# Performance work log

Hardware: AMD Instinct MI355X
Metric: run time of the kernel (lower is better)

## Reference

```python
import jax, jax.numpy as jnp
import numpy as np

F_IN, F_OUT, N_HEADS = 64, 256, 4
HEAD_DIM = F_OUT // N_HEADS


def setup_inputs() -> dict:
    key = jax.random.key(0)
    ks = jax.random.split(key, 9)
    s_in = 1.0 / np.sqrt(F_IN)
    s_out = 1.0 / np.sqrt(F_OUT)
    return {
        "x": jax.random.normal(ks[0], (4, 32, F_IN, 512), dtype=jnp.float32),
        "Wq": jax.random.normal(ks[1], (F_IN, F_OUT), dtype=jnp.float32) * s_in,
        "bq": jax.random.normal(ks[2], (F_OUT,), dtype=jnp.float32) * 0.01,
        "Wk": jax.random.normal(ks[3], (F_IN, F_OUT), dtype=jnp.float32) * s_in,
        "bk": jax.random.normal(ks[4], (F_OUT,), dtype=jnp.float32) * 0.01,
        "Wv": jax.random.normal(ks[5], (F_IN, F_OUT), dtype=jnp.float32) * s_in,
        "bv": jax.random.normal(ks[6], (F_OUT,), dtype=jnp.float32) * 0.01,
        "Wo": jax.random.normal(ks[7], (F_OUT, F_OUT), dtype=jnp.float32) * s_out,
        "bo": jax.random.normal(ks[8], (F_OUT,), dtype=jnp.float32) * 0.01,
    }


def reference(x, Wq, bq, Wk, bk, Wv, bv, Wo, bo):
    B, N, Fdim, T = x.shape
    xp = jnp.transpose(x, (0, 1, 3, 2))  # [B, N, T, F]
    q = xp @ Wq + bq  # [B, N, T, f_out]
    k = xp @ Wk + bk
    v = xp @ Wv + bv
    # split f_out into heads: [B, N, T, H, hd]
    q = q.reshape(B, N, T, N_HEADS, HEAD_DIM)
    k = k.reshape(B, N, T, N_HEADS, HEAD_DIM)
    v = v.reshape(B, N, T, N_HEADS, HEAD_DIM)
    scale = 1.0 / np.sqrt(HEAD_DIM)
    # full TxT score matrix per (batch, node, head), as in the original
    scores = jnp.einsum("bnqhd,bnkhd->bnhqk", q, k) * scale
    attn = jax.nn.softmax(scores, axis=-1)
    out = jnp.einsum("bnhqk,bnkhd->bnqhd", attn, v)  # [B, N, T, H, hd]
    out = out.reshape(B, N, T, F_OUT)  # head-concat along feature dim
    out = out @ Wo + bo  # fc_out; dropout is identity at inference
    return jnp.transpose(out, (0, 1, 3, 2))  # [B, N, f_out, T]
```

## Files before the change

### kernel.cpp

```cpp
#include <hip/hip_runtime.h>

constexpr int kT = 512;
constexpr int kF = 64;
constexpr int kC = 256;
constexpr int kH = 4;
constexpr int kHD = 64;
constexpr int kBN = 128;

typedef __attribute__((ext_vector_type(4))) float f32x4;
typedef __attribute__((ext_vector_type(8))) short s16x8;
typedef __attribute__((ext_vector_type(4))) unsigned int u32x4;

__device__ inline unsigned short f2bf(float f) {
  unsigned int u = __float_as_uint(f);
  u += 0x7fff + ((u >> 16) & 1);
  return (unsigned short)(u >> 16);
}

__device__ inline unsigned int cvt_pk(float a, float b) {
  unsigned int w;
  asm("v_cvt_pk_bf16_f32 %0, %1, %2" : "=v"(w) : "v"(a), "v"(b));
  return w;
}

__device__ inline float max3f(float a, float b, float c) {
  return fmaxf(fmaxf(a, b), c);
}

__device__ inline float exp2_hw(float x) {
  float r;
  asm("v_exp_f32 %0, %1" : "=v"(r) : "v"(x));
  return r;
}

__global__ __launch_bounds__(256) void k_prep(
    const float* __restrict__ Wq, const float* __restrict__ Wk,
    const float* __restrict__ Wv, const float* __restrict__ Wo,
    unsigned short* __restrict__ WB, unsigned short* __restrict__ WoT) {
  int i = blockIdx.x * 256 + threadIdx.x;
  const int total = 768 * 64 + 256 * 256;
  for (; i < total; i += gridDim.x * 256) {
    if (i < 768 * 64) {
      int c = i >> 6, f = i & 63;
      int arr = c >> 8, cc = c & 255;
      const float* W = (arr == 0) ? Wq : (arr == 1) ? Wk : Wv;
      WB[i] = f2bf(W[f * 256 + cc]);
    } else {
      int j = i - 768 * 64;
      int co = j >> 8, c = j & 255;
      WoT[j] = f2bf(Wo[c * 256 + co]);
    }
  }
}

__global__ __launch_bounds__(1024, 4) void k_fattn(
    const float* __restrict__ x, const unsigned short* __restrict__ WB,
    const float* __restrict__ bq, const float* __restrict__ bk,
    const float* __restrict__ bv, unsigned short* __restrict__ Aw) {
  __shared__ __align__(16) unsigned char smem[149504];
  unsigned char* Kl = smem;
  unsigned char* VtB = smem + 65536;
  unsigned char* xCb = smem + 131072;

  const int tid = threadIdx.x;
  const int bid = blockIdx.x;
  const int orig = (bid & 7) * 64 + (bid >> 3);
  const int lbn = orig >> 2;
  const int h = orig & 3;
  const int lane = tid & 63, wid = tid >> 6;
  const int lr = lane & 15, lg = lane >> 4;
  const int swz = (lr & 7) << 4;

  const float kQscale = 0.180336880111120426f;
  const unsigned short* WBq = WB + (size_t)(h * 64) * 64;
  const unsigned short* WBk = WB + (size_t)(256 + h * 64) * 64;
  const unsigned short* WBv = WB + (size_t)(512 + h * 64) * 64;

#define XFRAG(r, c) (const s16x8*)(xCb + (r) * 144 + \
    (((c) * 2) ^ ((((r) >> 2) & 7) << 4)))

  s16x8 qf[2][2];

  for (int tch = 0; tch < 4; ++tch) {
    __syncthreads();
    const float* xb = x + (size_t)lbn * kF * kT + tch * 128;
#pragma unroll
    for (int it = 0; it < 2; ++it) {
      int idx = tid + it * 1024;
      int f = idx >> 5, t4 = idx & 31;
      float4 v = *(const float4*)(xb + f * kT + t4 * 4);
      unsigned int wlo = cvt_pk(v.x, v.y);
      unsigned int whi = cvt_pk(v.z, v.w);
      const int fb = f * 2;
      const int colb = (fb & 15) | ((((fb >> 4) ^ (t4 & 7))) << 4);
      unsigned char* rp = xCb + (t4 * 4) * 144 + colb;
      *(unsigned short*)(rp + 0 * 144) = (unsigned short)wlo;
      *(unsigned short*)(rp + 1 * 144) = (unsigned short)(wlo >> 16);
      *(unsigned short*)(rp + 2 * 144) = (unsigned short)whi;
      *(unsigned short*)(rp + 3 * 144) = (unsigned short)(whi >> 16);
    }
    __syncthreads();

#pragma unroll
    for (int j = 0; j < 4; ++j) {
      const int tau = wid * 4 + j;
      const int isV = tau >> 5;
      const int tl = tau & 31;
      const int ct = tl >> 3, tt = tl & 7;
      const unsigned short* Wsrc = isV ? WBv : WBk;
      s16x8 af0 = *(const s16x8*)(Wsrc + (ct * 16 + lr) * 64 + lg * 8);
      s16x8 af1 = *(const s16x8*)(Wsrc + (ct * 16 + lr) * 64 + 32 + lg * 8);
      s16x8 bf0 = *XFRAG(tt * 16 + lr, lg * 8);
      s16x8 bf1 = *XFRAG(tt * 16 + lr, 32 + lg * 8);
      if (!isV) {
        f32x4 a = {0.f, 0.f, 0.f, 0.f};
        a = __builtin_amdgcn_mfma_f32_16x16x32_bf16(af0, bf0, a, 0, 0, 0);
        a = __builtin_amdgcn_mfma_f32_16x16x32_bf16(af1, bf1, a, 0, 0, 0);
        const int dbase = ct * 16 + lg * 4;
        const int t = tch * 128 + tt * 16 + lr;
        uint2 pk;
        pk.x = cvt_pk(a[0] + bk[h * 64 + dbase + 0],
                      a[1] + bk[h * 64 + dbase + 1]);
        pk.y = cvt_pk(a[2] + bk[h * 64 + dbase + 2],
                      a[3] + bk[h * 64 + dbase + 3]);
        *(uint2*)(Kl + ((t * 128 + dbase * 2) ^ ((t & 7) << 4))) = pk;
      } else {
        f32x4 a = {0.f, 0.f, 0.f, 0.f};
        a = __builtin_amdgcn_mfma_f32_16x16x32_bf16(bf0, af0, a, 0, 0, 0);
        a = __builtin_amdgcn_mfma_f32_16x16x32_bf16(bf1, af1, a, 0, 0, 0);
        const int d = ct * 16 + lr;
        const float bias = bv[h * 64 + d];
        const int t0 = tch * 128 + tt * 16 + lg * 4;
        const int pos0 = ((t0 >> 5) << 5) | (((t0 >> 2) & 3) << 3) |
                         (((t0 >> 4) & 1) << 2);
        uint2 pk;
        pk.x = cvt_pk(a[0] + bias, a[1] + bias);
        pk.y = cvt_pk(a[2] + bias, a[3] + bias);
        *(uint2*)(VtB + ((d * 1024 + pos0 * 2) ^ ((d & 7) << 4))) = pk;
      }
    }

    if ((wid >> 2) == tch) {
      f32x4 qa[2][4];
#pragma unroll
      for (int qt = 0; qt < 2; ++qt) {
        const int ttq = (wid & 3) * 2 + qt;
#pragma unroll
        for (int ct = 0; ct < 4; ++ct) {
          s16x8 af0 = *(const s16x8*)(WBq + (ct * 16 + lr) * 64 + lg * 8);
          s16x8 af1 = *(const s16x8*)(WBq + (ct * 16 + lr) * 64 + 32 + lg * 8);
          s16x8 bf0 = *XFRAG(ttq * 16 + lr, lg * 8);
          s16x8 bf1 = *XFRAG(ttq * 16 + lr, 32 + lg * 8);
          f32x4 a = {0.f, 0.f, 0.f, 0.f};
          a = __builtin_amdgcn_mfma_f32_16x16x32_bf16(af0, bf0, a, 0, 0, 0);
          a = __builtin_amdgcn_mfma_f32_16x16x32_bf16(af1, bf1, a, 0, 0, 0);
          const int dbase = ct * 16 + lg * 4;
#pragma unroll
          for (int r = 0; r < 4; ++r)
            a[r] = (a[r] + bq[h * 64 + dbase + r]) * kQscale;
          qa[qt][ct] = a;
        }
      }
      const int sel = lg >> 1;
#pragma unroll
      for (int qt = 0; qt < 2; ++qt)
#pragma unroll
        for (int half = 0; half < 2; ++half) {
          unsigned int w[4];
#pragma unroll
          for (int i2 = 0; i2 < 4; ++i2) {
            const int r0 = (i2 & 1) * 2;
            const int lgp = (lg & 1) * 2 + (i2 >> 1);
            const int src = lgp * 16 + lr;
            float loA = __shfl(qa[qt][half * 2 + 0][r0], src);
            float hiA = __shfl(qa[qt][half * 2 + 1][r0], src);
            float loB = __shfl(qa[qt][half * 2 + 0][r0 + 1], src);
            float hiB = __shfl(qa[qt][half * 2 + 1][r0 + 1], src);
            w[i2] = cvt_pk(sel ? hiA : loA, sel ? hiB : loB);
          }
          qf[qt][half] =
              __builtin_bit_cast(s16x8, (u32x4){w[0], w[1], w[2], w[3]});
        }
    }
  }
  __syncthreads();
#undef XFRAG

  unsigned short* Ab = Aw + (size_t)lbn * kT * kC + h * kHD;
  const int qbase = wid * 32;

  f32x4 o0[4] = {{0,0,0,0},{0,0,0,0},{0,0,0,0},{0,0,0,0}};
  f32x4 o1[4] = {{0,0,0,0},{0,0,0,0},{0,0,0,0},{0,0,0,0}};
  float m0 = -3e38f, m1 = -3e38f, l0 = 0.f, l1 = 0.f;

  const int koff = (lg * 16) ^ swz;
  const unsigned char* kp0 = Kl + lr * 128 + koff;
  const unsigned char* kp1 = Kl + lr * 128 + (koff ^ 64);
  const unsigned char* vp0 = VtB + lr * 1024 + ((lg * 16) ^ swz);
  const unsigned char* vp1 = VtB + lr * 1024 + (((lg * 16) ^ 64) ^ swz);

  unsigned int w0[8], w1[8];

#define SOFTMAX_QT(sa, m, l, o, w)                                            \
  {                                                                           \
    float g0 = max3f(sa[0][0], sa[0][1], sa[0][2]);                           \
    float g1 = max3f(sa[0][3], sa[1][0], sa[1][1]);                           \
    float g2 = max3f(sa[1][2], sa[1][3], sa[2][0]);                           \
    float g3 = max3f(sa[2][1], sa[2][2], sa[2][3]);                           \
    float g4 = max3f(sa[3][0], sa[3][1], sa[3][2]);                           \
    float tm = fmaxf(max3f(g0, g1, g2), max3f(g3, g4, sa[3][3]));             \
    if (__any(tm > m + 8.0f)) {                                               \
      tm = fmaxf(tm, __shfl_xor(tm, 16));                                     \
      tm = fmaxf(tm, __shfl_xor(tm, 32));                                     \
      float mn = fmaxf(m, tm);                                                \
      float al = exp2_hw(m - mn);                                             \
      m = mn;                                                                 \
      l *= al;                                                                \
      float aq0 = __shfl(al, (lane & 48) | (lg * 4 + 0));                     \
      float aq1 = __shfl(al, (lane & 48) | (lg * 4 + 1));                     \
      float aq2 = __shfl(al, (lane & 48) | (lg * 4 + 2));                     \
      float aq3 = __shfl(al, (lane & 48) | (lg * 4 + 3));                     \
      _Pragma("unroll")                                                       \
      for (int dt = 0; dt < 4; ++dt) {                                        \
        o[dt][0] *= aq0; o[dt][1] *= aq1;                                     \
        o[dt][2] *= aq2; o[dt][3] *= aq3;                                     \
      }                                                                       \
    }                                                                         \
    _Pragma("unroll")                                                         \
    for (int s = 0; s < 4; ++s) {                                             \
      float e0 = exp2_hw(sa[s][0] - m);                                       \
      float e1 = exp2_hw(sa[s][1] - m);                                       \
      float e2 = exp2_hw(sa[s][2] - m);                                       \
      float e3 = exp2_hw(sa[s][3] - m);                                       \
      l += (e0 + e1) + (e2 + e3);                                             \
      w[2*s]   = cvt_pk(e0, e1);                                              \
      w[2*s+1] = cvt_pk(e2, e3);                                              \
    }                                                                         \
  }

  for (int kc = 0; kc < 8; ++kc) {
    f32x4 sa0[4], sa1[4];
#pragma unroll
    for (int s = 0; s < 4; ++s) {
      s16x8 kf0 = *(const s16x8*)(kp0 + s * 2048);
      s16x8 kf1 = *(const s16x8*)(kp1 + s * 2048);
      f32x4 z0 = {0.f, 0.f, 0.f, 0.f};
      z0 = __builtin_amdgcn_mfma_f32_16x16x32_bf16(kf0, qf[0][0], z0, 0, 0, 0);
      z0 = __builtin_amdgcn_mfma_f32_16x16x32_bf16(kf1, qf[0][1], z0, 0, 0, 0);
      sa0[s] = z0;
      f32x4 z1 = {0.f, 0.f, 0.f, 0.f};
      z1 = __builtin_amdgcn_mfma_f32_16x16x32_bf16(kf0, qf[1][0], z1, 0, 0, 0);
      z1 = __builtin_amdgcn_mfma_f32_16x16x32_bf16(kf1, qf[1][1], z1, 0, 0, 0);
      sa1[s] = z1;
    }
    kp0 += 8192;
    kp1 += 8192;

    s16x8 vb0[4], vb1[4];
#pragma unroll
    for (int dt = 0; dt < 4; ++dt) {
      vb0[dt] = *(const s16x8*)(vp0 + dt * 16384);
      vb1[dt] = *(const s16x8*)(vp1 + dt * 16384);
    }
    vp0 += 128;
    vp1 += 128;

    SOFTMAX_QT(sa0, m0, l0, o0, w0)
    SOFTMAX_QT(sa1, m1, l1, o1, w1)

    s16x8 pa00 = __builtin_bit_cast(s16x8, (u32x4){w0[0], w0[1], w0[2], w0[3]});
    s16x8 pa01 = __builtin_bit_cast(s16x8, (u32x4){w0[4], w0[5], w0[6], w0[7]});
    s16x8 pa10 = __builtin_bit_cast(s16x8, (u32x4){w1[0], w1[1], w1[2], w1[3]});
    s16x8 pa11 = __builtin_bit_cast(s16x8, (u32x4){w1[4], w1[5], w1[6], w1[7]});

#pragma unroll
    for (int dt = 0; dt < 4; ++dt) {
      o0[dt] = __builtin_amdgcn_mfma_f32_16x16x32_bf16(pa00, vb0[dt], o0[dt], 0, 0, 0);
      o1[dt] = __builtin_amdgcn_mfma_f32_16x16x32_bf16(pa10, vb0[dt], o1[dt], 0, 0, 0);
    }
#pragma unroll
    for (int dt = 0; dt < 4; ++dt) {
      o0[dt] = __builtin_amdgcn_mfma_f32_16x16x32_bf16(pa01, vb1[dt], o0[dt], 0, 0, 0);
      o1[dt] = __builtin_amdgcn_mfma_f32_16x16x32_bf16(pa11, vb1[dt], o1[dt], 0, 0, 0);
    }
  }
#undef SOFTMAX_QT

#pragma unroll
  for (int qt = 0; qt < 2; ++qt) {
    float l = (qt == 0) ? l0 : l1;
    f32x4* o = (qt == 0) ? o0 : o1;
    float l2 = l + __shfl_xor(l, 16);
    float lr4 = l2 + __shfl_xor(l2, 32);
    float li0 = 1.0f / __shfl(lr4, (lane & 48) | (lg * 4 + 0));
    float li1 = 1.0f / __shfl(lr4, (lane & 48) | (lg * 4 + 1));
    float li2 = 1.0f / __shfl(lr4, (lane & 48) | (lg * 4 + 2));
    float li3 = 1.0f / __shfl(lr4, (lane & 48) | (lg * 4 + 3));
    const int qb = qbase + qt * 16;
#pragma unroll
    for (int r = 0; r < 4; ++r) {
      float li = (r == 0) ? li0 : (r == 1) ? li1 : (r == 2) ? li2 : li3;
      unsigned short* orow = Ab + (size_t)(qb + lg * 4 + r) * kC;
      unsigned int wa = cvt_pk(o[0][r] * li, o[1][r] * li);
      unsigned int wb = cvt_pk(o[2][r] * li, o[3][r] * li);
      orow[0 * 16 + lr] = (unsigned short)wa;
      orow[1 * 16 + lr] = (unsigned short)(wa >> 16);
      orow[2 * 16 + lr] = (unsigned short)wb;
      orow[3 * 16 + lr] = (unsigned short)(wb >> 16);
    }
  }
}

__global__ __launch_bounds__(512) void k_proj(
    const unsigned short* __restrict__ Aw, const unsigned short* __restrict__ WoT,
    const float* __restrict__ bo, float* __restrict__ out) {
  __shared__ __align__(16) unsigned char Al[128 * 512];

  const int tid = threadIdx.x;
  const int lbn = blockIdx.x >> 2;
  const int tch = blockIdx.x & 3;
  const int t0 = tch * 128;

  const uint4* Asrc = (const uint4*)(Aw + ((size_t)lbn * kT + t0) * kC);
#pragma unroll
  for (int i = 0; i < 8; ++i) {
    int idx = tid + i * 512;
    int trow = idx >> 5, cc = idx & 31;
    *(uint4*)(Al + ((trow * 512 + cc * 16) ^ ((trow & 7) << 4))) = Asrc[idx];
  }
  __syncthreads();

  const int lane = tid & 63, wid = tid >> 6;
  const int lr = lane & 15, lg = lane >> 4;
  const int swz = (lr & 7) << 4;
  const int tb = (wid >> 2) * 64;
  const int cob = (wid & 3) * 64;

  float* ob = out + (size_t)lbn * kC * kT;

  for (int ci = 0; ci < 4; ++ci) {
    const int co0 = cob + ci * 16;
    s16x8 af[8];
#pragma unroll
    for (int kc = 0; kc < 8; ++kc)
      af[kc] = *(const s16x8*)(WoT + (size_t)(co0 + lr) * 256 + kc * 32 + lg * 8);
    float b4[4];
#pragma unroll
    for (int r = 0; r < 4; ++r) b4[r] = bo[co0 + lg * 4 + r];

#pragma unroll
    for (int tj = 0; tj < 4; ++tj) {
      const unsigned char* ap = Al + (tb + tj * 16 + lr) * 512;
      f32x4 acc = {0.f, 0.f, 0.f, 0.f};
#pragma unroll
      for (int kc = 0; kc < 8; ++kc) {
        s16x8 bfr = *(const s16x8*)(ap + ((kc * 64 + lg * 16) ^ swz));
        acc = __builtin_amdgcn_mfma_f32_16x16x32_bf16(af[kc], bfr, acc, 0, 0, 0);
      }
      int t = t0 + tb + tj * 16 + lr;
#pragma unroll
      for (int r = 0; r < 4; ++r)
        ob[(size_t)(co0 + lg * 4 + r) * kT + t] = acc[r] + b4[r];
    }
  }
}

extern "C" void kernel_launch(void* const* d_in, const int* in_sizes, int n_in,
                              void* d_out, int out_size, void* d_ws, size_t ws_size,
                              hipStream_t stream) {
  const float* x  = (const float*)d_in[0];
  const float* Wq = (const float*)d_in[1];
  const float* bq = (const float*)d_in[2];
  const float* Wk = (const float*)d_in[3];
  const float* bk = (const float*)d_in[4];
  const float* Wv = (const float*)d_in[5];
  const float* bv = (const float*)d_in[6];
  const float* Wo = (const float*)d_in[7];
  const float* bo = (const float*)d_in[8];
  float* out = (float*)d_out;

  const size_t wElems = 768 * 64 + 256 * 256;
  const size_t aBytes = (size_t)kBN * kT * kC * 2;
  if (ws_size < wElems * 2 + aBytes) return;

  unsigned short* WB  = (unsigned short*)d_ws;
  unsigned short* WoT = WB + 768 * 64;
  unsigned short* A   = WB + wElems;

  k_prep<<<dim3(448), dim3(256), 0, stream>>>(Wq, Wk, Wv, Wo, WB, WoT);
  k_fattn<<<dim3(kBN * kH), dim3(1024), 0, stream>>>(x, WB, bq, bk, bv, A);
  k_proj<<<dim3(kBN * 4), dim3(512), 0, stream>>>(A, WoT, bo, out);
}
```

Baseline: 120.7 us.

## Overlap attention chunks with K/V projection and prefetch x tiles

Q is now computed up front by each wave straight from global x, without going through the shared x tile. The attention loop over key chunks is interleaved with the per-tch K/V projection, so chunks already written to LDS are consumed while later chunks are still being produced. The next x tile is prefetched into registers one iteration ahead. This aims to hide projection and global-load latency behind attention MFMA work, at the cost of strided uncoalesced global reads for Q and higher register pressure.

```diff
diff --git a/kernel.cpp b/kernel.cpp
--- a/kernel.cpp
+++ b/kernel.cpp
@@ -75,29 +75,194 @@
   const unsigned short* WBq = WB + (size_t)(h * 64) * 64;
   const unsigned short* WBk = WB + (size_t)(256 + h * 64) * 64;
   const unsigned short* WBv = WB + (size_t)(512 + h * 64) * 64;
+  const float* xb0 = x + (size_t)lbn * kF * kT;
 
 #define XFRAG(r, c) (const s16x8*)(xCb + (r) * 144 + \
     (((c) * 2) ^ ((((r) >> 2) & 7) << 4)))
 
+  const int qbase = wid * 32;
+
   s16x8 qf[2][2];
+  {
+    f32x4 qa[2][4];
+#pragma unroll
+    for (int qt = 0; qt < 2; ++qt) {
+      const int tq = qbase + qt * 16 + lr;
+      s16x8 bfr[2];
+#pragma unroll
+      for (int kk = 0; kk < 2; ++kk) {
+        unsigned int wv[4];
+#pragma unroll
+        for (int jp = 0; jp < 4; ++jp) {
+          float fa = xb0[(size_t)(kk * 32 + lg * 8 + 2 * jp) * kT + tq];
+          float fb = xb0[(size_t)(kk * 32 + lg * 8 + 2 * jp + 1) * kT + tq];
+          wv[jp] = cvt_pk(fa, fb);
+        }
+        bfr[kk] = __builtin_bit_cast(s16x8, (u32x4){wv[0], wv[1], wv[2], wv[3]});
+      }
+#pragma unroll
+      for (int ct = 0; ct < 4; ++ct) {
+        s16x8 af0 = *(const s16x8*)(WBq + (ct * 16 + lr) * 64 + lg * 8);
+        s16x8 af1 = *(const s16x8*)(WBq + (ct * 16 + lr) * 64 + 32 + lg * 8);
+        f32x4 a = {0.f, 0.f, 0.f, 0.f};
+        a = __builtin_amdgcn_mfma_f32_16x16x32_bf16(af0, bfr[0], a, 0, 0, 0);
+        a = __builtin_amdgcn_mfma_f32_16x16x32_bf16(af1, bfr[1], a, 0, 0, 0);
+        const int dbase = ct * 16 + lg * 4;
+#pragma unroll
+        for (int r = 0; r < 4; ++r)
+          a[r] = (a[r] + bq[h * 64 + dbase + r]) * kQscale;
+        qa[qt][ct] = a;
+      }
+    }
+    const int sel = lg >> 1;
+#pragma unroll
+    for (int qt = 0; qt < 2; ++qt)
+#pragma unroll
+      for (int half = 0; half < 2; ++half) {
+        unsigned int w[4];
+#pragma unroll
+        for (int i2 = 0; i2 < 4; ++i2) {
+          const int r0 = (i2 & 1) * 2;
+          const int lgp = (lg & 1) * 2 + (i2 >> 1);
+          const int src = lgp * 16 + lr;
+          float loA = __shfl(qa[qt][half * 2 + 0][r0], src);
+          float hiA = __shfl(qa[qt][half * 2 + 1][r0], src);
+          float loB = __shfl(qa[qt][half * 2 + 0][r0 + 1], src);
+          float hiB = __shfl(qa[qt][half * 2 + 1][r0 + 1], src);
+          w[i2] = cvt_pk(sel ? hiA : loA, sel ? hiB : loB);
+        }
+        qf[qt][half] =
+            __builtin_bit_cast(s16x8, (u32x4){w[0], w[1], w[2], w[3]});
+      }
+  }
+
+  unsigned short* Ab = Aw + (size_t)lbn * kT * kC + h * kHD;
+  f32x4 o0[4] = {{0,0,0,0},{0,0,0,0},{0,0,0,0},{0,0,0,0}};
+  f32x4 o1[4] = {{0,0,0,0},{0,0,0,0},{0,0,0,0},{0,0,0,0}};
+  float m0 = -3e38f, m1 = -3e38f, l0 = 0.f, l1 = 0.f;
+  unsigned int w0[8], w1[8];
+
+  const int koff = (lg * 16) ^ swz;
+  const unsigned char* kb0 = Kl + lr * 128 + koff;
+  const unsigned char* kb1 = Kl + lr * 128 + (koff ^ 64);
+  const unsigned char* vbp0 = VtB + lr * 1024 + ((lg * 16) ^ swz);
+  const unsigned char* vbp1 = VtB + lr * 1024 + (((lg * 16) ^ 64) ^ swz);
+
+#define SOFTMAX_QT(sa, m, l, o, w)                                            \
+  {                                                                           \
+    float g0 = max3f(sa[0][0], sa[0][1], sa[0][2]);                           \
+    float g1 = max3f(sa[0][3], sa[1][0], sa[1][1]);                           \
+    float g2 = max3f(sa[1][2], sa[1][3], sa[2][0]);                           \
+    float g3 = max3f(sa[2][1], sa[2][2], sa[2][3]);                           \
+    float g4 = max3f(sa[3][0], sa[3][1], sa[3][2]);                           \
+    float tm = fmaxf(max3f(g0, g1, g2), max3f(g3, g4, sa[3][3]));             \
+    if (__any(tm > m + 8.0f)) {                                               \
+      tm = fmaxf(tm, __shfl_xor(tm, 16));                                     \
+      tm = fmaxf(tm, __shfl_xor(tm, 32));                                     \
+      float mn = fmaxf(m, tm);                                                \
+      float al = exp2_hw(m - mn);                                             \
+      m = mn;                                                                 \
+      l *= al;                                                                \
+      float aq0 = __shfl(al, (lane & 48) | (lg * 4 + 0));                     \
+      float aq1 = __shfl(al, (lane & 48) | (lg * 4 + 1));                     \
+      float aq2 = __shfl(al, (lane & 48) | (lg * 4 + 2));                     \
+      float aq3 = __shfl(al, (lane & 48) | (lg * 4 + 3));                     \
+      _Pragma("unroll")                                                       \
+      for (int dt = 0; dt < 4; ++dt) {                                        \
+        o[dt][0] *= aq0; o[dt][1] *= aq1;                                     \
+        o[dt][2] *= aq2; o[dt][3] *= aq3;                                     \
+      }                                                                       \
+    }                                                                         \
+    _Pragma("unroll")                                                         \
+    for (int s = 0; s < 4; ++s) {                                             \
+      float e0 = exp2_hw(sa[s][0] - m);                                       \
+      float e1 = exp2_hw(sa[s][1] - m);                                       \
+      float e2 = exp2_hw(sa[s][2] - m);                                       \
+      float e3 = exp2_hw(sa[s][3] - m);                                       \
+      l += (e0 + e1) + (e2 + e3);                                             \
+      w[2*s]   = cvt_pk(e0, e1);                                              \
+      w[2*s+1] = cvt_pk(e2, e3);                                              \
+    }                                                                         \
+  }
+
+#define ATTN_KC(kc)                                                           \
+  {                                                                           \
+    const unsigned char* kp0_ = kb0 + (kc) * 8192;                            \
+    const unsigned char* kp1_ = kb1 + (kc) * 8192;                            \
+    f32x4 sa0[4], sa1[4];                                                     \
+    _Pragma("unroll")                                                         \
+    for (int s = 0; s < 4; ++s) {                                             \
+      s16x8 kf0 = *(const s16x8*)(kp0_ + s * 2048);                           \
+      s16x8 kf1 = *(const s16x8*)(kp1_ + s * 2048);                           \
+      f32x4 z0 = {0.f, 0.f, 0.f, 0.f};                                        \
+      z0 = __builtin_amdgcn_mfma_f32_16x16x32_bf16(kf0, qf[0][0], z0, 0,0,0); \
+      z0 = __builtin_amdgcn_mfma_f32_16x16x32_bf16(kf1, qf[0][1], z0, 0,0,0); \
+      sa0[s] = z0;                                                            \
+      f32x4 z1 = {0.f, 0.f, 0.f, 0.f};                                        \
+      z1 = __builtin_amdgcn_mfma_f32_16x16x32_bf16(kf0, qf[1][0], z1, 0,0,0); \
+      z1 = __builtin_amdgcn_mfma_f32_16x16x32_bf16(kf1, qf[1][1], z1, 0,0,0); \
+      sa1[s] = z1;                                                            \
+    }                                                                         \
+    s16x8 vv0[4], vv1[4];                                                     \
+    _Pragma("unroll")                                                         \
+    for (int dt = 0; dt < 4; ++dt) {                                          \
+      vv0[dt] = *(const s16x8*)(vbp0 + (kc) * 128 + dt * 16384);              \
+      vv1[dt] = *(const s16x8*)(vbp1 + (kc) * 128 + dt * 16384);              \
+    }                                                                         \
+    SOFTMAX_QT(sa0, m0, l0, o0, w0)                                           \
+    SOFTMAX_QT(sa1, m1, l1, o1, w1)                                           \
+    s16x8 pa00 = __builtin_bit_cast(s16x8, (u32x4){w0[0],w0[1],w0[2],w0[3]}); \
+    s16x8 pa01 = __builtin_bit_cast(s16x8, (u32x4){w0[4],w0[5],w0[6],w0[7]}); \
+    s16x8 pa10 = __builtin_bit_cast(s16x8, (u32x4){w1[0],w1[1],w1[2],w1[3]}); \
+    s16x8 pa11 = __builtin_bit_cast(s16x8, (u32x4){w1[4],w1[5],w1[6],w1[7]}); \
+    _Pragma("unroll")                                                         \
+    for (int dt = 0; dt < 4; ++dt) {                                          \
+      o0[dt] = __builtin_amdgcn_mfma_f32_16x16x32_bf16(pa00, vv0[dt], o0[dt], 0,0,0); \
+      o1[dt] = __builtin_amdgcn_mfma_f32_16x16x32_bf16(pa10, vv0[dt], o1[dt], 0,0,0); \
+    }                                                                         \
+    _Pragma("unroll")                                                         \
+    for (int dt = 0; dt < 4; ++dt) {                                          \
+      o0[dt] = __builtin_amdgcn_mfma_f32_16x16x32_bf16(pa01, vv1[dt], o0[dt], 0,0,0); \
+      o1[dt] = __builtin_amdgcn_mfma_f32_16x16x32_bf16(pa11, vv1[dt], o1[dt], 0,0,0); \
+    }                                                                         \
+  }
+
+  const int sf0 = tid >> 5;
+  const int st4 = tid & 31;
+  const int sf1 = (tid + 1024) >> 5;
+
+  float4 pf0 = *(const float4*)(xb0 + (size_t)sf0 * kT + st4 * 4);
+  float4 pf1 = *(const float4*)(xb0 + (size_t)sf1 * kT + st4 * 4);
 
   for (int tch = 0; tch < 4; ++tch) {
     __syncthreads();
-    const float* xb = x + (size_t)lbn * kF * kT + tch * 128;
-#pragma unroll
-    for (int it = 0; it < 2; ++it) {
-      int idx = tid + it * 1024;
-      int f = idx >> 5, t4 = idx & 31;
-      float4 v = *(const float4*)(xb + f * kT + t4 * 4);
-      unsigned int wlo = cvt_pk(v.x, v.y);
-      unsigned int whi = cvt_pk(v.z, v.w);
-      const int fb = f * 2;
-      const int colb = (fb & 15) | ((((fb >> 4) ^ (t4 & 7))) << 4);
-      unsigned char* rp = xCb + (t4 * 4) * 144 + colb;
+
+    {
+      unsigned int wlo = cvt_pk(pf0.x, pf0.y);
+      unsigned int whi = cvt_pk(pf0.z, pf0.w);
+      int colb = ((sf0 * 2) & 15) | (((((sf0 * 2) >> 4) ^ (st4 & 7))) << 4);
+      unsigned char* rp = xCb + (st4 * 4) * 144 + colb;
       *(unsigned short*)(rp + 0 * 144) = (unsigned short)wlo;
       *(unsigned short*)(rp + 1 * 144) = (unsigned short)(wlo >> 16);
       *(unsigned short*)(rp + 2 * 144) = (unsigned short)whi;
       *(unsigned short*)(rp + 3 * 144) = (unsigned short)(whi >> 16);
+      wlo = cvt_pk(pf1.x, pf1.y);
+      whi = cvt_pk(pf1.z, pf1.w);
+      colb = ((sf1 * 2) & 15) | (((((sf1 * 2) >> 4) ^ (st4 & 7))) << 4);
+      rp = xCb + (st4 * 4) * 144 + colb;
+      *(unsigned short*)(rp + 0 * 144) = (unsigned short)wlo;
+      *(unsigned short*)(rp + 1 * 144) = (unsigned short)(wlo >> 16);
+      *(unsigned short*)(rp + 2 * 144) = (unsigned short)whi;
+      *(unsigned short*)(rp + 3 * 144) = (unsigned short)(whi >> 16);
+    }
+    if (tch < 3) {
+      const float* xb = xb0 + (tch + 1) * 128;
+      pf0 = *(const float4*)(xb + (size_t)sf0 * kT + st4 * 4);
+      pf1 = *(const float4*)(xb + (size_t)sf1 * kT + st4 * 4);
+    }
+    if (tch > 0) {
+      ATTN_KC(2 * tch - 2)
+      ATTN_KC(2 * tch - 1)
     }
     __syncthreads();
 
@@ -139,152 +304,14 @@
         *(uint2*)(VtB + ((d * 1024 + pos0 * 2) ^ ((d & 7) << 4))) = pk;
       }
     }
-
-    if ((wid >> 2) == tch) {
-      f32x4 qa[2][4];
-#pragma unroll
-      for (int qt = 0; qt < 2; ++qt) {
-        const int ttq = (wid & 3) * 2 + qt;
-#pragma unroll
-        for (int ct = 0; ct < 4; ++ct) {
-          s16x8 af0 = *(const s16x8*)(WBq + (ct * 16 + lr) * 64 + lg * 8);
-          s16x8 af1 = *(const s16x8*)(WBq + (ct * 16 + lr) * 64 + 32 + lg * 8);
-          s16x8 bf0 = *XFRAG(ttq * 16 + lr, lg * 8);
-          s16x8 bf1 = *XFRAG(ttq * 16 + lr, 32 + lg * 8);
-          f32x4 a = {0.f, 0.f, 0.f, 0.f};
-          a = __builtin_amdgcn_mfma_f32_16x16x32_bf16(af0, bf0, a, 0, 0, 0);
-          a = __builtin_amdgcn_mfma_f32_16x16x32_bf16(af1, bf1, a, 0, 0, 0);
-          const int dbase = ct * 16 + lg * 4;
-#pragma unroll
-          for (int r = 0; r < 4; ++r)
-            a[r] = (a[r] + bq[h * 64 + dbase + r]) * kQscale;
-          qa[qt][ct] = a;
-        }
-      }
-      const int sel = lg >> 1;
-#pragma unroll
-      for (int qt = 0; qt < 2; ++qt)
-#pragma unroll
-        for (int half = 0; half < 2; ++half) {
-          unsigned int w[4];
-#pragma unroll
-          for (int i2 = 0; i2 < 4; ++i2) {
-            const int r0 = (i2 & 1) * 2;
-            const int lgp = (lg & 1) * 2 + (i2 >> 1);
-            const int src = lgp * 16 + lr;
-            float loA = __shfl(qa[qt][half * 2 + 0][r0], src);
-            float hiA = __shfl(qa[qt][half * 2 + 1][r0], src);
-            float loB = __shfl(qa[qt][half * 2 + 0][r0 + 1], src);
-            float hiB = __shfl(qa[qt][half * 2 + 1][r0 + 1], src);
-            w[i2] = cvt_pk(sel ? hiA : loA, sel ? hiB : loB);
-          }
-          qf[qt][half] =
-              __builtin_bit_cast(s16x8, (u32x4){w[0], w[1], w[2], w[3]});
-        }
-    }
   }
   __syncthreads();
+
+  ATTN_KC(6)
+  ATTN_KC(7)
+#undef ATTN_KC
+#undef SOFTMAX_QT
 #undef XFRAG
-
-  unsigned short* Ab = Aw + (size_t)lbn * kT * kC + h * kHD;
-  const int qbase = wid * 32;
-
-  f32x4 o0[4] = {{0,0,0,0},{0,0,0,0},{0,0,0,0},{0,0,0,0}};
-  f32x4 o1[4] = {{0,0,0,0},{0,0,0,0},{0,0,0,0},{0,0,0,0}};
-  float m0 = -3e38f, m1 = -3e38f, l0 = 0.f, l1 = 0.f;
-
-  const int koff = (lg * 16) ^ swz;
-  const unsigned char* kp0 = Kl + lr * 128 + koff;
-  const unsigned char* kp1 = Kl + lr * 128 + (koff ^ 64);
-  const unsigned char* vp0 = VtB + lr * 1024 + ((lg * 16) ^ swz);
-  const unsigned char* vp1 = VtB + lr * 1024 + (((lg * 16) ^ 64) ^ swz);
-
-  unsigned int w0[8], w1[8];
-
-#define SOFTMAX_QT(sa, m, l, o, w)                                            \
-  {                                                                           \
-    float g0 = max3f(sa[0][0], sa[0][1], sa[0][2]);                           \
-    float g1 = max3f(sa[0][3], sa[1][0], sa[1][1]);                           \
-    float g2 = max3f(sa[1][2], sa[1][3], sa[2][0]);                           \
-    float g3 = max3f(sa[2][1], sa[2][2], sa[2][3]);                           \
-    float g4 = max3f(sa[3][0], sa[3][1], sa[3][2]);                           \
-    float tm = fmaxf(max3f(g0, g1, g2), max3f(g3, g4, sa[3][3]));             \
-    if (__any(tm > m + 8.0f)) {                                               \
-      tm = fmaxf(tm, __shfl_xor(tm, 16));                                     \
-      tm = fmaxf(tm, __shfl_xor(tm, 32));                                     \
-      float mn = fmaxf(m, tm);                                                \
-      float al = exp2_hw(m - mn);                                             \
-      m = mn;                                                                 \
-      l *= al;                                                                \
-      float aq0 = __shfl(al, (lane & 48) | (lg * 4 + 0));                     \
-      float aq1 = __shfl(al, (lane & 48) | (lg * 4 + 1));                     \
-      float aq2 = __shfl(al, (lane & 48) | (lg * 4 + 2));                     \
-      float aq3 = __shfl(al, (lane & 48) | (lg * 4 + 3));                     \
-      _Pragma("unroll")                                                       \
-      for (int dt = 0; dt < 4; ++dt) {                                        \
-        o[dt][0] *= aq0; o[dt][1] *= aq1;                                     \
-        o[dt][2] *= aq2; o[dt][3] *= aq3;                                     \
-      }                                                                       \
-    }                                                                         \
-    _Pragma("unroll")                                                         \
-    for (int s = 0; s < 4; ++s) {                                             \
-      float e0 = exp2_hw(sa[s][0] - m);                                       \
-      float e1 = exp2_hw(sa[s][1] - m);                                       \
-      float e2 = exp2_hw(sa[s][2] - m);                                       \
-      float e3 = exp2_hw(sa[s][3] - m);                                       \
-      l += (e0 + e1) + (e2 + e3);                                             \
-      w[2*s]   = cvt_pk(e0, e1);                                              \
-      w[2*s+1] = cvt_pk(e2, e3);                                              \
-    }                                                                         \
-  }
-
-  for (int kc = 0; kc < 8; ++kc) {
-    f32x4 sa0[4], sa1[4];
-#pragma unroll
-    for (int s = 0; s < 4; ++s) {
-      s16x8 kf0 = *(const s16x8*)(kp0 + s * 2048);
-      s16x8 kf1 = *(const s16x8*)(kp1 + s * 2048);
-      f32x4 z0 = {0.f, 0.f, 0.f, 0.f};
-      z0 = __builtin_amdgcn_mfma_f32_16x16x32_bf16(kf0, qf[0][0], z0, 0, 0, 0);
-      z0 = __builtin_amdgcn_mfma_f32_16x16x32_bf16(kf1, qf[0][1], z0, 0, 0, 0);
-      sa0[s] = z0;
-      f32x4 z1 = {0.f, 0.f, 0.f, 0.f};
-      z1 = __builtin_amdgcn_mfma_f32_16x16x32_bf16(kf0, qf[1][0], z1, 0, 0, 0);
-      z1 = __builtin_amdgcn_mfma_f32_16x16x32_bf16(kf1, qf[1][1], z1, 0, 0, 0);
-      sa1[s] = z1;
-    }
-    kp0 += 8192;
-    kp1 += 8192;
-
-    s16x8 vb0[4], vb1[4];
-#pragma unroll
-    for (int dt = 0; dt < 4; ++dt) {
-      vb0[dt] = *(const s16x8*)(vp0 + dt * 16384);
-      vb1[dt] = *(const s16x8*)(vp1 + dt * 16384);
-    }
-    vp0 += 128;
-    vp1 += 128;
-
-    SOFTMAX_QT(sa0, m0, l0, o0, w0)
-    SOFTMAX_QT(sa1, m1, l1, o1, w1)
-
-    s16x8 pa00 = __builtin_bit_cast(s16x8, (u32x4){w0[0], w0[1], w0[2], w0[3]});
-    s16x8 pa01 = __builtin_bit_cast(s16x8, (u32x4){w0[4], w0[5], w0[6], w0[7]});
-    s16x8 pa10 = __builtin_bit_cast(s16x8, (u32x4){w1[0], w1[1], w1[2], w1[3]});
-    s16x8 pa11 = __builtin_bit_cast(s16x8, (u32x4){w1[4], w1[5], w1[6], w1[7]});
-
-#pragma unroll
-    for (int dt = 0; dt < 4; ++dt) {
-      o0[dt] = __builtin_amdgcn_mfma_f32_16x16x32_bf16(pa00, vb0[dt], o0[dt], 0, 0, 0);
-      o1[dt] = __builtin_amdgcn_mfma_f32_16x16x32_bf16(pa10, vb0[dt], o1[dt], 0, 0, 0);
-    }
-#pragma unroll
-    for (int dt = 0; dt < 4; ++dt) {
-      o0[dt] = __builtin_amdgcn_mfma_f32_16x16x32_bf16(pa01, vb1[dt], o0[dt], 0, 0, 0);
-      o1[dt] = __builtin_amdgcn_mfma_f32_16x16x32_bf16(pa11, vb1[dt], o1[dt], 0, 0, 0);
-    }
-  }
-#undef SOFTMAX_QT
 
 #pragma unroll
   for (int qt = 0; qt < 2; ++qt) {
```

After: 200.7 us. 66.4% more time.

## Split attention blocks by query half and stream K/V in two key halves

Applied to the files above, without the earlier changes.

The fused attention kernel now launches twice as many 512-thread blocks, each handling half of the queries for one (batch-node, head). K and V are projected in two 256-key halves into smaller shared buffers, and attention runs over each half before the next is built. Q is computed straight from global x instead of staging it through shared memory. Shared memory per block is roughly halved, which raises occupancy, but every query-half block recomputes the full K and V projection, doubling that work and the x reads, and adds syncs between halves.

```diff
diff --git a/kernel.cpp b/kernel.cpp
--- a/kernel.cpp
+++ b/kernel.cpp
@@ -53,20 +53,21 @@
   }
 }
 
-__global__ __launch_bounds__(1024, 4) void k_fattn(
+__global__ __launch_bounds__(512, 4) void k_fattn(
     const float* __restrict__ x, const unsigned short* __restrict__ WB,
     const float* __restrict__ bq, const float* __restrict__ bk,
     const float* __restrict__ bv, unsigned short* __restrict__ Aw) {
-  __shared__ __align__(16) unsigned char smem[149504];
+  __shared__ __align__(16) unsigned char smem[73728];
   unsigned char* Kl = smem;
-  unsigned char* VtB = smem + 65536;
-  unsigned char* xCb = smem + 131072;
+  unsigned char* VtB = smem + 32768;
+  unsigned char* xCb = smem + 65536;
 
   const int tid = threadIdx.x;
   const int bid = blockIdx.x;
-  const int orig = (bid & 7) * 64 + (bid >> 3);
-  const int lbn = orig >> 2;
-  const int h = orig & 3;
+  const int orig = (bid & 7) * 128 + (bid >> 3);
+  const int lbn = orig >> 3;
+  const int h = (orig >> 1) & 3;
+  const int qhalf = orig & 1;
   const int lane = tid & 63, wid = tid >> 6;
   const int lr = lane & 15, lg = lane >> 4;
   const int swz = (lr & 7) << 4;
@@ -75,131 +76,73 @@
   const unsigned short* WBq = WB + (size_t)(h * 64) * 64;
   const unsigned short* WBk = WB + (size_t)(256 + h * 64) * 64;
   const unsigned short* WBv = WB + (size_t)(512 + h * 64) * 64;
-
-#define XFRAG(r, c) (const s16x8*)(xCb + (r) * 144 + \
-    (((c) * 2) ^ ((((r) >> 2) & 7) << 4)))
+  const float* xb0 = x + (size_t)lbn * kF * kT;
 
   s16x8 qf[2][2];
-
-  for (int tch = 0; tch < 4; ++tch) {
-    __syncthreads();
-    const float* xb = x + (size_t)lbn * kF * kT + tch * 128;
-#pragma unroll
-    for (int it = 0; it < 2; ++it) {
-      int idx = tid + it * 1024;
-      int f = idx >> 5, t4 = idx & 31;
-      float4 v = *(const float4*)(xb + f * kT + t4 * 4);
-      unsigned int wlo = cvt_pk(v.x, v.y);
-      unsigned int whi = cvt_pk(v.z, v.w);
-      const int fb = f * 2;
-      const int colb = (fb & 15) | ((((fb >> 4) ^ (t4 & 7))) << 4);
-      unsigned char* rp = xCb + (t4 * 4) * 144 + colb;
-      *(unsigned short*)(rp + 0 * 144) = (unsigned short)wlo;
-      *(unsigned short*)(rp + 1 * 144) = (unsigned short)(wlo >> 16);
-      *(unsigned short*)(rp + 2 * 144) = (unsigned short)whi;
-      *(unsigned short*)(rp + 3 * 144) = (unsigned short)(whi >> 16);
-    }
-    __syncthreads();
-
-#pragma unroll
-    for (int j = 0; j < 4; ++j) {
-      const int tau = wid * 4 + j;
-      const int isV = tau >> 5;
-      const int tl = tau & 31;
-      const int ct = tl >> 3, tt = tl & 7;
-      const unsigned short* Wsrc = isV ? WBv : WBk;
-      s16x8 af0 = *(const s16x8*)(Wsrc + (ct * 16 + lr) * 64 + lg * 8);
-      s16x8 af1 = *(const s16x8*)(Wsrc + (ct * 16 + lr) * 64 + 32 + lg * 8);
-      s16x8 bf0 = *XFRAG(tt * 16 + lr, lg * 8);
-      s16x8 bf1 = *XFRAG(tt * 16 + lr, 32 + lg * 8);
-      if (!isV) {
+  {
+    f32x4 qa[2][4];
+#pragma unroll
+    for (int qt = 0; qt < 2; ++qt) {
+      const int tq = qhalf * 256 + wid * 32 + qt * 16 + lr;
+      s16x8 bfr[2];
+#pragma unroll
+      for (int kk = 0; kk < 2; ++kk) {
+        unsigned int wv[4];
+#pragma unroll
+        for (int jp = 0; jp < 4; ++jp) {
+          float fa = xb0[(size_t)(kk * 32 + lg * 8 + 2 * jp) * kT + tq];
+          float fb = xb0[(size_t)(kk * 32 + lg * 8 + 2 * jp + 1) * kT + tq];
+          wv[jp] = cvt_pk(fa, fb);
+        }
+        bfr[kk] = __builtin_bit_cast(s16x8, (u32x4){wv[0], wv[1], wv[2], wv[3]});
+      }
+#pragma unroll
+      for (int ct = 0; ct < 4; ++ct) {
+        s16x8 af0 = *(const s16x8*)(WBq + (ct * 16 + lr) * 64 + lg * 8);
+        s16x8 af1 = *(const s16x8*)(WBq + (ct * 16 + lr) * 64 + 32 + lg * 8);
         f32x4 a = {0.f, 0.f, 0.f, 0.f};
-        a = __builtin_amdgcn_mfma_f32_16x16x32_bf16(af0, bf0, a, 0, 0, 0);
-        a = __builtin_amdgcn_mfma_f32_16x16x32_bf16(af1, bf1, a, 0, 0, 0);
+        a = __builtin_amdgcn_mfma_f32_16x16x32_bf16(af0, bfr[0], a, 0, 0, 0);
+        a = __builtin_amdgcn_mfma_f32_16x16x32_bf16(af1, bfr[1], a, 0, 0, 0);
         const int dbase = ct * 16 + lg * 4;
-        const int t = tch * 128 + tt * 16 + lr;
-        uint2 pk;
-        pk.x = cvt_pk(a[0] + bk[h * 64 + dbase + 0],
-                      a[1] + bk[h * 64 + dbase + 1]);
-        pk.y = cvt_pk(a[2] + bk[h * 64 + dbase + 2],
-                      a[3] + bk[h * 64 + dbase + 3]);
-        *(uint2*)(Kl + ((t * 128 + dbase * 2) ^ ((t & 7) << 4))) = pk;
-      } else {
-        f32x4 a = {0.f, 0.f, 0.f, 0.f};
-        a = __builtin_amdgcn_mfma_f32_16x16x32_bf16(bf0, af0, a, 0, 0, 0);
-        a = __builtin_amdgcn_mfma_f32_16x16x32_bf16(bf1, af1, a, 0, 0, 0);
-        const int d = ct * 16 + lr;
-        const float bias = bv[h * 64 + d];
-        const int t0 = tch * 128 + tt * 16 + lg * 4;
-        const int pos0 = ((t0 >> 5) << 5) | (((t0 >> 2) & 3) << 3) |
-                         (((t0 >> 4) & 1) << 2);
-        uint2 pk;
-        pk.x = cvt_pk(a[0] + bias, a[1] + bias);
-        pk.y = cvt_pk(a[2] + bias, a[3] + bias);
-        *(uint2*)(VtB + ((d * 1024 + pos0 * 2) ^ ((d & 7) << 4))) = pk;
-      }
-    }
-
-    if ((wid >> 2) == tch) {
-      f32x4 qa[2][4];
-#pragma unroll
-      for (int qt = 0; qt < 2; ++qt) {
-        const int ttq = (wid & 3) * 2 + qt;
-#pragma unroll
-        for (int ct = 0; ct < 4; ++ct) {
-          s16x8 af0 = *(const s16x8*)(WBq + (ct * 16 + lr) * 64 + lg * 8);
-          s16x8 af1 = *(const s16x8*)(WBq + (ct * 16 + lr) * 64 + 32 + lg * 8);
-          s16x8 bf0 = *XFRAG(ttq * 16 + lr, lg * 8);
-          s16x8 bf1 = *XFRAG(ttq * 16 + lr, 32 + lg * 8);
-          f32x4 a = {0.f, 0.f, 0.f, 0.f};
-          a = __builtin_amdgcn_mfma_f32_16x16x32_bf16(af0, bf0, a, 0, 0, 0);
-          a = __builtin_amdgcn_mfma_f32_16x16x32_bf16(af1, bf1, a, 0, 0, 0);
-          const int dbase = ct * 16 + lg * 4;
-#pragma unroll
-          for (int r = 0; r < 4; ++r)
-            a[r] = (a[r] + bq[h * 64 + dbase + r]) * kQscale;
-          qa[qt][ct] = a;
+#pragma unroll
+        for (int r = 0; r < 4; ++r)
+          a[r] = (a[r] + bq[h * 64 + dbase + r]) * kQscale;
+        qa[qt][ct] = a;
+      }
+    }
+    const int sel = lg >> 1;
+#pragma unroll
+    for (int qt = 0; qt < 2; ++qt)
+#pragma unroll
+      for (int half = 0; half < 2; ++half) {
+        unsigned int w[4];
+#pragma unroll
+        for (int i2 = 0; i2 < 4; ++i2) {
+          const int r0 = (i2 & 1) * 2;
+          const int lgp = (lg & 1) * 2 + (i2 >> 1);
+          const int src = lgp * 16 + lr;
+          float loA = __shfl(qa[qt][half * 2 + 0][r0], src);
+          float hiA = __shfl(qa[qt][half * 2 + 1][r0], src);
+          float loB = __shfl(qa[qt][half * 2 + 0][r0 + 1], src);
+          float hiB = __shfl(qa[qt][half * 2 + 1][r0 + 1], src);
+          w[i2] = cvt_pk(sel ? hiA : loA, sel ? hiB : loB);
         }
-      }
-      const int sel = lg >> 1;
-#pragma unroll
-      for (int qt = 0; qt < 2; ++qt)
-#pragma unroll
-        for (int half = 0; half < 2; ++half) {
-          unsigned int w[4];
-#pragma unroll
-          for (int i2 = 0; i2 < 4; ++i2) {
-            const int r0 = (i2 & 1) * 2;
-            const int lgp = (lg & 1) * 2 + (i2 >> 1);
-            const int src = lgp * 16 + lr;
-            float loA = __shfl(qa[qt][half * 2 + 0][r0], src);
-            float hiA = __shfl(qa[qt][half * 2 + 1][r0], src);
-            float loB = __shfl(qa[qt][half * 2 + 0][r0 + 1], src);
-            float hiB = __shfl(qa[qt][half * 2 + 1][r0 + 1], src);
-            w[i2] = cvt_pk(sel ? hiA : loA, sel ? hiB : loB);
-          }
-          qf[qt][half] =
-              __builtin_bit_cast(s16x8, (u32x4){w[0], w[1], w[2], w[3]});
-        }
-    }
-  }
-  __syncthreads();
-#undef XFRAG
+        qf[qt][half] =
+            __builtin_bit_cast(s16x8, (u32x4){w[0], w[1], w[2], w[3]});
+      }
+  }
 
   unsigned short* Ab = Aw + (size_t)lbn * kT * kC + h * kHD;
-  const int qbase = wid * 32;
-
   f32x4 o0[4] = {{0,0,0,0},{0,0,0,0},{0,0,0,0},{0,0,0,0}};
   f32x4 o1[4] = {{0,0,0,0},{0,0,0,0},{0,0,0,0},{0,0,0,0}};
   float m0 = -3e38f, m1 = -3e38f, l0 = 0.f, l1 = 0.f;
+  unsigned int w0[8], w1[8];
 
   const int koff = (lg * 16) ^ swz;
-  const unsigned char* kp0 = Kl + lr * 128 + koff;
-  const unsigned char* kp1 = Kl + lr * 128 + (koff ^ 64);
-  const unsigned char* vp0 = VtB + lr * 1024 + ((lg * 16) ^ swz);
-  const unsigned char* vp1 = VtB + lr * 1024 + (((lg * 16) ^ 64) ^ swz);
-
-  unsigned int w0[8], w1[8];
+  const unsigned char* kb0 = Kl + lr * 128 + koff;
+  const unsigned char* kb1 = Kl + lr * 128 + (koff ^ 64);
+  const unsigned char* vbp0 = VtB + lr * 512 + ((lg * 16) ^ swz);
+  const unsigned char* vbp1 = VtB + lr * 512 + (((lg * 16) ^ 64) ^ swz);
 
 #define SOFTMAX_QT(sa, m, l, o, w)                                            \
   {                                                                           \
@@ -238,50 +181,109 @@
     }                                                                         \
   }
 
-  for (int kc = 0; kc < 8; ++kc) {
-    f32x4 sa0[4], sa1[4];
-#pragma unroll
-    for (int s = 0; s < 4; ++s) {
-      s16x8 kf0 = *(const s16x8*)(kp0 + s * 2048);
-      s16x8 kf1 = *(const s16x8*)(kp1 + s * 2048);
-      f32x4 z0 = {0.f, 0.f, 0.f, 0.f};
-      z0 = __builtin_amdgcn_mfma_f32_16x16x32_bf16(kf0, qf[0][0], z0, 0, 0, 0);
-      z0 = __builtin_amdgcn_mfma_f32_16x16x32_bf16(kf1, qf[0][1], z0, 0, 0, 0);
-      sa0[s] = z0;
-      f32x4 z1 = {0.f, 0.f, 0.f, 0.f};
-      z1 = __builtin_amdgcn_mfma_f32_16x16x32_bf16(kf0, qf[1][0], z1, 0, 0, 0);
-      z1 = __builtin_amdgcn_mfma_f32_16x16x32_bf16(kf1, qf[1][1], z1, 0, 0, 0);
-      sa1[s] = z1;
-    }
-    kp0 += 8192;
-    kp1 += 8192;
-
-    s16x8 vb0[4], vb1[4];
-#pragma unroll
-    for (int dt = 0; dt < 4; ++dt) {
-      vb0[dt] = *(const s16x8*)(vp0 + dt * 16384);
-      vb1[dt] = *(const s16x8*)(vp1 + dt * 16384);
-    }
-    vp0 += 128;
-    vp1 += 128;
-
-    SOFTMAX_QT(sa0, m0, l0, o0, w0)
-    SOFTMAX_QT(sa1, m1, l1, o1, w1)
-
-    s16x8 pa00 = __builtin_bit_cast(s16x8, (u32x4){w0[0], w0[1], w0[2], w0[3]});
-    s16x8 pa01 = __builtin_bit_cast(s16x8, (u32x4){w0[4], w0[5], w0[6], w0[7]});
-    s16x8 pa10 = __builtin_bit_cast(s16x8, (u32x4){w1[0], w1[1], w1[2], w1[3]});
-    s16x8 pa11 = __builtin_bit_cast(s16x8, (u32x4){w1[4], w1[5], w1[6], w1[7]});
-
-#pragma unroll
-    for (int dt = 0; dt < 4; ++dt) {
-      o0[dt] = __builtin_amdgcn_mfma_f32_16x16x32_bf16(pa00, vb0[dt], o0[dt], 0, 0, 0);
-      o1[dt] = __builtin_amdgcn_mfma_f32_16x16x32_bf16(pa10, vb0[dt], o1[dt], 0, 0, 0);
-    }
-#pragma unroll
-    for (int dt = 0; dt < 4; ++dt) {
-      o0[dt] = __builtin_amdgcn_mfma_f32_16x16x32_bf16(pa01, vb1[dt], o0[dt], 0, 0, 0);
-      o1[dt] = __builtin_amdgcn_mfma_f32_16x16x32_bf16(pa11, vb1[dt], o1[dt], 0, 0, 0);
+  for (int half = 0; half < 2; ++half) {
+    for (int sc = 0; sc < 4; ++sc) {
+      __syncthreads();
+      const float* xb = xb0 + half * 256 + sc * 64;
+#pragma unroll
+      for (int it = 0; it < 2; ++it) {
+        int idx = tid + it * 512;
+        int f = idx >> 4, t4 = idx & 15;
+        float4 v = *(const float4*)(xb + (size_t)f * kT + t4 * 4);
+        unsigned int wlo = cvt_pk(v.x, v.y);
+        unsigned int whi = cvt_pk(v.z, v.w);
+        const int colb = (f * 2) ^ ((t4 & 7) << 4);
+        unsigned char* rp = xCb + (t4 * 4) * 128 + colb;
+        *(unsigned short*)(rp + 0 * 128) = (unsigned short)wlo;
+        *(unsigned short*)(rp + 1 * 128) = (unsigned short)(wlo >> 16);
+        *(unsigned short*)(rp + 2 * 128) = (unsigned short)whi;
+        *(unsigned short*)(rp + 3 * 128) = (unsigned short)(whi >> 16);
+      }
+      __syncthreads();
+
+#pragma unroll
+      for (int j = 0; j < 4; ++j) {
+        const int tau = wid * 4 + j;
+        const int isV = tau >> 4;
+        const int tl = tau & 15;
+        const int ct = tl >> 2, tt = tl & 3;
+        const unsigned short* Wsrc = isV ? WBv : WBk;
+        s16x8 af0 = *(const s16x8*)(Wsrc + (ct * 16 + lr) * 64 + lg * 8);
+        s16x8 af1 = *(const s16x8*)(Wsrc + (ct * 16 + lr) * 64 + 32 + lg * 8);
+        const int xr = tt * 16 + lr;
+        s16x8 bf0 = *(const s16x8*)(xCb + xr * 128 +
+                                    ((lg * 16) ^ (((xr >> 2) & 7) << 4)));
+        s16x8 bf1 = *(const s16x8*)(xCb + xr * 128 +
+                                    ((64 + lg * 16) ^ (((xr >> 2) & 7) << 4)));
+        if (!isV) {
+          f32x4 a = {0.f, 0.f, 0.f, 0.f};
+          a = __builtin_amdgcn_mfma_f32_16x16x32_bf16(af0, bf0, a, 0, 0, 0);
+          a = __builtin_amdgcn_mfma_f32_16x16x32_bf16(af1, bf1, a, 0, 0, 0);
+          const int dbase = ct * 16 + lg * 4;
+          const int t = sc * 64 + tt * 16 + lr;
+          uint2 pk;
+          pk.x = cvt_pk(a[0] + bk[h * 64 + dbase + 0],
+                        a[1] + bk[h * 64 + dbase + 1]);
+          pk.y = cvt_pk(a[2] + bk[h * 64 + dbase + 2],
+                        a[3] + bk[h * 64 + dbase + 3]);
+          *(uint2*)(Kl + ((t * 128 + dbase * 2) ^ ((t & 7) << 4))) = pk;
+        } else {
+          f32x4 a = {0.f, 0.f, 0.f, 0.f};
+          a = __builtin_amdgcn_mfma_f32_16x16x32_bf16(bf0, af0, a, 0, 0, 0);
+          a = __builtin_amdgcn_mfma_f32_16x16x32_bf16(bf1, af1, a, 0, 0, 0);
+          const int d = ct * 16 + lr;
+          const float bias = bv[h * 64 + d];
+          const int t0 = sc * 64 + tt * 16 + lg * 4;
+          const int pos0 = ((t0 >> 5) << 5) | (((t0 >> 2) & 3) << 3) |
+                           (((t0 >> 4) & 1) << 2);
+          uint2 pk;
+          pk.x = cvt_pk(a[0] + bias, a[1] + bias);
+          pk.y = cvt_pk(a[2] + bias, a[3] + bias);
+          *(uint2*)(VtB + ((d * 512 + pos0 * 2) ^ ((d & 7) << 4))) = pk;
+        }
+      }
+    }
+    __syncthreads();
+
+    for (int kc = 0; kc < 4; ++kc) {
+      const unsigned char* kp0_ = kb0 + kc * 8192;
+      const unsigned char* kp1_ = kb1 + kc * 8192;
+      f32x4 sa0[4], sa1[4];
+#pragma unroll
+      for (int s = 0; s < 4; ++s) {
+        s16x8 kf0 = *(const s16x8*)(kp0_ + s * 2048);
+        s16x8 kf1 = *(const s16x8*)(kp1_ + s * 2048);
+        f32x4 z0 = {0.f, 0.f, 0.f, 0.f};
+        z0 = __builtin_amdgcn_mfma_f32_16x16x32_bf16(kf0, qf[0][0], z0, 0,0,0);
+        z0 = __builtin_amdgcn_mfma_f32_16x16x32_bf16(kf1, qf[0][1], z0, 0,0,0);
+        sa0[s] = z0;
+        f32x4 z1 = {0.f, 0.f, 0.f, 0.f};
+        z1 = __builtin_amdgcn_mfma_f32_16x16x32_bf16(kf0, qf[1][0], z1, 0,0,0);
+        z1 = __builtin_amdgcn_mfma_f32_16x16x32_bf16(kf1, qf[1][1], z1, 0,0,0);
+        sa1[s] = z1;
+      }
+      s16x8 vv0[4], vv1[4];
+#pragma unroll
+      for (int dt = 0; dt < 4; ++dt) {
+        vv0[dt] = *(const s16x8*)(vbp0 + kc * 128 + dt * 8192);
+        vv1[dt] = *(const s16x8*)(vbp1 + kc * 128 + dt * 8192);
+      }
+      SOFTMAX_QT(sa0, m0, l0, o0, w0)
+      SOFTMAX_QT(sa1, m1, l1, o1, w1)
+      s16x8 pa00 = __builtin_bit_cast(s16x8, (u32x4){w0[0],w0[1],w0[2],w0[3]});
+      s16x8 pa01 = __builtin_bit_cast(s16x8, (u32x4){w0[4],w0[5],w0[6],w0[7]});
+      s16x8 pa10 = __builtin_bit_cast(s16x8, (u32x4){w1[0],w1[1],w1[2],w1[3]});
+      s16x8 pa11 = __builtin_bit_cast(s16x8, (u32x4){w1[4],w1[5],w1[6],w1[7]});
+#pragma unroll
+      for (int dt = 0; dt < 4; ++dt) {
+        o0[dt] = __builtin_amdgcn_mfma_f32_16x16x32_bf16(pa00, vv0[dt], o0[dt], 0,0,0);
+        o1[dt] = __builtin_amdgcn_mfma_f32_16x16x32_bf16(pa10, vv0[dt], o1[dt], 0,0,0);
+      }
+#pragma unroll
+      for (int dt = 0; dt < 4; ++dt) {
+        o0[dt] = __builtin_amdgcn_mfma_f32_16x16x32_bf16(pa01, vv1[dt], o0[dt], 0,0,0);
+        o1[dt] = __builtin_amdgcn_mfma_f32_16x16x32_bf16(pa11, vv1[dt], o1[dt], 0,0,0);
+      }
     }
   }
 #undef SOFTMAX_QT
@@ -296,7 +298,7 @@
     float li1 = 1.0f / __shfl(lr4, (lane & 48) | (lg * 4 + 1));
     float li2 = 1.0f / __shfl(lr4, (lane & 48) | (lg * 4 + 2));
     float li3 = 1.0f / __shfl(lr4, (lane & 48) | (lg * 4 + 3));
-    const int qb = qbase + qt * 16;
+    const int qb = qhalf * 256 + wid * 32 + qt * 16;
 #pragma unroll
     for (int r = 0; r < 4; ++r) {
       float li = (r == 0) ? li0 : (r == 1) ? li1 : (r == 2) ? li2 : li3;
@@ -388,6 +390,6 @@
   unsigned short* A   = WB + wElems;
 
   k_prep<<<dim3(448), dim3(256), 0, stream>>>(Wq, Wk, Wv, Wo, WB, WoT);
-  k_fattn<<<dim3(kBN * kH), dim3(1024), 0, stream>>>(x, WB, bq, bk, bv, A);
+  k_fattn<<<dim3(kBN * kH * 2), dim3(512), 0, stream>>>(x, WB, bq, bk, bv, A);
   k_proj<<<dim3(kBN * 4), dim3(512), 0, stream>>>(A, WoT, bo, out);
 }
```

Result: slower. 158.8 us (+31.6%).
